# Performance work log

Measured on AMD Instinct MI355X. Metric: run time of the kernel, lower is better.

The kernel has to match this reference:

```python
import jax, jax.numpy as jnp
import numpy as np

B, N, IN_DIM, DIM, HEADS, P = 4, 2048, 256, 512, 8, 16
DH = DIM // HEADS            # 64
SCALE = DH ** -0.5


def setup_inputs() -> dict:
    key = jax.random.key(0)
    ks = jax.random.split(key, 8)
    def w(k, shape, s=0.02):
        return jax.random.normal(k, shape, dtype=jnp.float32) * s
    return {
        "x": jax.random.normal(ks[0], (B, N, IN_DIM), dtype=jnp.float32),
        "w_qkv": w(ks[1], (IN_DIM, 3 * DIM)),
        "b_qkv": jnp.zeros((3 * DIM,), jnp.float32),
        "w_in": w(ks[2], (P, P)),
        "b_in": jnp.zeros((P,), jnp.float32),
        "w_out": w(ks[3], (P, P)),
        "b_out": jnp.zeros((P,), jnp.float32),
        "w_merge": w(ks[4], (DIM, DIM)),
        "b_merge": jnp.zeros((DIM,), jnp.float32),
        "w_proj": w(ks[5], (DIM + IN_DIM, DIM)),
        "b_proj": jnp.zeros((DIM,), jnp.float32),
        "H": 64,
        "W": 32,
    }


def reference(x, w_qkv, b_qkv, w_in, b_in, w_out, b_out,
              w_merge, b_merge, w_proj, b_proj, H, W):
    b, n, _ = x.shape
    qkv = x @ w_qkv + b_qkv                      # [b, n, 3*DIM]
    q, k, v = jnp.split(qkv, 3, axis=-1)
    def to_heads(t):
        return t.reshape(b, n, HEADS, DH).transpose(0, 2, 1, 3)  # [b, h, n, d]
    q, k, v = to_heads(q), to_heads(k), to_heads(v)
    # Original splits heads into h/v halves and runs two attentions, then
    # concats along the head axis. Softmax is per-head, so this is exactly
    # one batched multi-head attention with head order preserved.
    attn = jax.nn.softmax(jnp.einsum('bhnd,bhmd->bhnm', q, k) * SCALE, axis=-1)
    out = jnp.einsum('bhnm,bhmd->bhnd', attn, v)
    out = out.transpose(0, 2, 1, 3).reshape(b, n, DIM)
    out = out @ w_merge + b_merge
    # IBPP branch: view channels as [P, P] grid, linear-SiLU-linear on last dim
    xr = x.reshape(b, n, P, P)
    ib = jax.nn.silu(xr @ w_in + b_in) @ w_out + b_out
    ib = ib.reshape(b, n, IN_DIM)
    # proj (dropout p=0 -> identity)
    return jnp.concatenate([out, ib], axis=-1) @ w_proj + b_proj
```

## Files before the change

kernel.cpp:

```cpp
#include <hip/hip_runtime.h>


typedef unsigned short u16;
typedef unsigned int u32;
typedef __bf16 bf16x8 __attribute__((ext_vector_type(8)));
typedef u16 su16x8 __attribute__((ext_vector_type(8)));
typedef u16 su16x4 __attribute__((ext_vector_type(4)));
typedef u32 u32x4 __attribute__((ext_vector_type(4)));
typedef float f32x4 __attribute__((ext_vector_type(4)));

__device__ __forceinline__ u16 f2bf(float f) {
  union { __bf16 h; u16 u; } v;
  v.h = (__bf16)f;
  return v.u;
}

__device__ __forceinline__ float fexp2(float x) {
#if __has_builtin(__builtin_amdgcn_exp2f)
  return __builtin_amdgcn_exp2f(x);
#else
  return __expf(x * 0.6931471805599453f);
#endif
}

__device__ __forceinline__ f32x4 zero4() {
  f32x4 v = {0.f, 0.f, 0.f, 0.f};
  return v;
}

__device__ __forceinline__ f32x4 mfma16(bf16x8 a, bf16x8 b, f32x4 c) {
  return __builtin_amdgcn_mfma_f32_16x16x32_bf16(a, b, c, 0, 0, 0);
}

__global__ __launch_bounds__(256) void prep_kernel(
    const float* __restrict__ w_qkv, const float* __restrict__ w_merge,
    const float* __restrict__ w_proj, const float* __restrict__ b_merge,
    const float* __restrict__ b_proj, u16* __restrict__ wqkvT,
    u16* __restrict__ wptT, u16* __restrict__ wcombT, u16* __restrict__ wmb,
    float* __restrict__ biasc) {
  int blk = blockIdx.x, tid = threadIdx.x;
  if (blk < 192) {
    const float* src;
    int lsrc, ldd, r0, c0;
    u16* dst;
    if (blk < 96) {
      src = w_qkv; lsrc = 1536; dst = wqkvT; ldd = 256;
      r0 = (blk & 3) * 64; c0 = (blk >> 2) * 64;
    } else if (blk < 160) {
      int b2 = blk - 96;
      src = w_proj; lsrc = 512; dst = wptT; ldd = 512;
      r0 = (b2 & 7) * 64; c0 = (b2 >> 3) * 64;
    } else {
      int b2 = blk - 160;
      src = w_proj + 512 * 512; lsrc = 512; dst = wcombT + 512; ldd = 768;
      r0 = (b2 & 3) * 64; c0 = (b2 >> 2) * 64;
    }
    __shared__ __align__(16) u16 Ts[64 * 68];
    int rr = tid >> 4, cc4 = (tid & 15) * 4;
#pragma unroll
    for (int rep = 0; rep < 4; ++rep) {
      int r = rr + rep * 16;
      float4 v = *(const float4*)&src[(size_t)(r0 + r) * lsrc + c0 + cc4];
      su16x4 pk = {f2bf(v.x), f2bf(v.y), f2bf(v.z), f2bf(v.w)};
      *(su16x4*)&Ts[r * 68 + cc4] = pk;
    }
    __syncthreads();
    int c = tid & 63, seg = tid >> 6;
    u16 tmp[16];
#pragma unroll
    for (int k = 0; k < 16; ++k) tmp[k] = Ts[(seg * 16 + k) * 68 + c];
    *(su16x8*)&dst[(size_t)(c0 + c) * ldd + r0 + seg * 16] = *(su16x8*)tmp;
    *(su16x8*)&dst[(size_t)(c0 + c) * ldd + r0 + seg * 16 + 8] =
        *(su16x8*)(tmp + 8);
  } else if (blk < 256) {
    int b2 = blk - 192;
#pragma unroll
    for (int rep = 0; rep < 4; ++rep) {
      int i = b2 * 4096 + rep * 1024 + tid * 4;
      float4 v = *(const float4*)&w_merge[i];
      su16x4 pk = {f2bf(v.x), f2bf(v.y), f2bf(v.z), f2bf(v.w)};
      *(su16x4*)&wmb[i] = pk;
    }
  } else {
    int col0 = (blk - 256) * 16;
    __shared__ float red[16][17];
    int kr = tid >> 4, cc = tid & 15;
    float s = 0.f;
#pragma unroll 4
    for (int j = 0; j < 32; ++j) {
      int k = kr + j * 16;
      s += b_merge[k] * w_proj[(size_t)k * 512 + col0 + cc];
    }
    red[kr][cc] = s;
    __syncthreads();
    if (kr == 0) {
      float a = b_proj[col0 + cc];
#pragma unroll
      for (int t = 0; t < 16; ++t) a += red[t][cc];
      biasc[col0 + cc] = a;
    }
  }
}

__global__ __launch_bounds__(256) void ib_kernel(
    const float* __restrict__ x, const float* __restrict__ w_in,
    const float* __restrict__ b_in, const float* __restrict__ w_out,
    const float* __restrict__ b_out, u16* __restrict__ xb,
    u16* __restrict__ catb) {
  __shared__ float wi[256], wo[256], bi[16], bo[16];
  __shared__ float xs[16][260];
  __shared__ float hs[16][260];
  int tid = threadIdx.x;
  wi[tid] = w_in[tid];
  wo[tid] = w_out[tid];
  if (tid < 16) { bi[tid] = b_in[tid]; bo[tid] = b_out[tid]; }
  size_t blkoff = (size_t)blockIdx.x * 4096;
#pragma unroll
  for (int i = 0; i < 4; ++i) {
    int f = (tid + i * 256) * 4;
    float4 v = *(const float4*)&x[blkoff + f];
    int tok = f >> 8, p = f & 255;
    *(float4*)&xs[tok][p] = v;
    su16x4 pk = {f2bf(v.x), f2bf(v.y), f2bf(v.z), f2bf(v.w)};
    *(su16x4*)&xb[blkoff + f] = pk;
  }
  __syncthreads();
  int t = tid >> 4, p2 = tid & 15;
#pragma unroll
  for (int p1 = 0; p1 < 16; ++p1) {
    float a = bi[p2];
#pragma unroll
    for (int k = 0; k < 16; ++k) a += xs[t][p1 * 16 + k] * wi[k * 16 + p2];
    hs[t][p1 * 16 + p2] = a / (1.f + __expf(-a));
  }
  __syncthreads();
  size_t tok = (size_t)blockIdx.x * 16 + t;
#pragma unroll
  for (int p1 = 0; p1 < 16; ++p1) {
    float o = bo[p2];
#pragma unroll
    for (int j = 0; j < 16; ++j) o += hs[t][p1 * 16 + j] * wo[j * 16 + p2];
    catb[tok * 768 + 512 + p1 * 16 + p2] = f2bf(o);
  }
}

template <int TM, int TN, int WGM, int WGN, int OUTMODE>
__global__ __launch_bounds__(256) void gemm_bt(
    const u16* __restrict__ A, int lda, const u16* __restrict__ BT, int ldb,
    int kcount, const float* __restrict__ bias, void* __restrict__ Co, int ldc,
    int scaleQ) {
  constexpr int NROWS = TM + TN;
  constexpr int NLD = NROWS / 64;
  constexpr int MT = TM / WGM / 16;
  constexpr int NT = TN / WGN / 16;
  __shared__ __align__(16) u16 S[NROWS * 40];
  int tid = threadIdx.x;
  int lane = tid & 63, wave = tid >> 6;
  int c = lane & 15, g4 = lane >> 4;
  int m0 = blockIdx.y * TM, n0 = blockIdx.x * TN;
  int wm = (wave / WGN) * (TM / WGM), wn = (wave % WGN) * (TN / WGN);
  f32x4 acc[MT][NT];
#pragma unroll
  for (int a = 0; a < MT; ++a)
#pragma unroll
    for (int b = 0; b < NT; ++b) acc[a][b] = zero4();

  su16x8 pre[NLD];
#pragma unroll
  for (int t = 0; t < NLD; ++t) {
    int gsl = t * 256 + tid;
    int row = gsl >> 2, kg = gsl & 3;
    const u16* p = row < TM ? &A[(size_t)(m0 + row) * lda + kg * 8]
                            : &BT[(size_t)(n0 + row - TM) * ldb + kg * 8];
    pre[t] = *(const su16x8*)p;
  }

  for (int kb = 0; kb < kcount; kb += 32) {
    __syncthreads();
#pragma unroll
    for (int t = 0; t < NLD; ++t) {
      int gsl = t * 256 + tid;
      int row = gsl >> 2, kg = gsl & 3;
      *(su16x8*)&S[row * 40 + kg * 8] = pre[t];
    }
    __syncthreads();
    if (kb + 32 < kcount) {
#pragma unroll
      for (int t = 0; t < NLD; ++t) {
        int gsl = t * 256 + tid;
        int row = gsl >> 2, kg = gsl & 3;
        const u16* p =
            row < TM ? &A[(size_t)(m0 + row) * lda + kb + 32 + kg * 8]
                     : &BT[(size_t)(n0 + row - TM) * ldb + kb + 32 + kg * 8];
        pre[t] = *(const su16x8*)p;
      }
    }
    bf16x8 af[MT], bf[NT];
#pragma unroll
    for (int mt = 0; mt < MT; ++mt)
      af[mt] = *(const bf16x8*)&S[(wm + mt * 16 + c) * 40 + g4 * 8];
#pragma unroll
    for (int nt = 0; nt < NT; ++nt)
      bf[nt] = *(const bf16x8*)&S[(TM + wn + nt * 16 + c) * 40 + g4 * 8];
#pragma unroll
    for (int mt = 0; mt < MT; ++mt)
#pragma unroll
      for (int nt = 0; nt < NT; ++nt)
        acc[mt][nt] = mfma16(af[mt], bf[nt], acc[mt][nt]);
  }

  if (OUTMODE == 0) {
    float* Cf = (float*)Co;
#pragma unroll
    for (int nt = 0; nt < NT; ++nt) {
      int col = n0 + wn + nt * 16 + c;
      float bv = bias ? bias[col] : 0.f;
#pragma unroll
      for (int mt = 0; mt < MT; ++mt)
#pragma unroll
        for (int i = 0; i < 4; ++i)
          Cf[(size_t)(m0 + wm + mt * 16 + g4 * 4 + i) * ldc + col] =
              acc[mt][nt][i] + bv;
    }
  } else if (OUTMODE == 2) {
    u16* C16 = (u16*)Co;
#pragma unroll
    for (int nt = 0; nt < NT; ++nt)
#pragma unroll
      for (int mt = 0; mt < MT; ++mt)
#pragma unroll
        for (int i = 0; i < 4; ++i)
          C16[(size_t)(m0 + wm + mt * 16 + g4 * 4 + i) * ldc + n0 + wn +
              nt * 16 + c] = f2bf(acc[mt][nt][i]);
  } else {
    u16* C16 = (u16*)Co;
    u16* Cs = S;
    __syncthreads();
#pragma unroll
    for (int half = 0; half < 2; ++half) {
      if ((wave >> 1) == half) {
#pragma unroll
        for (int nt = 0; nt < NT; ++nt) {
          int col = n0 + wn + nt * 16 + c;
          float bv = bias ? bias[col] : 0.f;
          float sc = (scaleQ && col < 512) ? 0.18033688011112042f : 1.f;
#pragma unroll
          for (int mt = 0; mt < MT; ++mt)
#pragma unroll
            for (int i = 0; i < 4; ++i)
              Cs[(mt * 16 + g4 * 4 + i) * 136 + wn + nt * 16 + c] =
                  f2bf((acc[mt][nt][i] + bv) * sc);
        }
      }
      __syncthreads();
      {
        int row = tid >> 2;
#pragma unroll
        for (int t = 0; t < 4; ++t) {
          int gr = (tid & 3) + t * 4;
          u32x4 v = *(const u32x4*)&Cs[row * 136 + gr * 8];
          *(u32x4*)&C16[(size_t)(m0 + half * 64 + row) * ldc + n0 + gr * 8] = v;
        }
      }
      __syncthreads();
    }
  }
}

__global__ __launch_bounds__(256) void attn_kernel(
    const u16* __restrict__ qkvb, u16* __restrict__ catb) {
  __shared__ __align__(16) u16 Ks[9216];
  __shared__ __align__(16) u16 Vs[8704];
  __shared__ __align__(16) u16 Ps[8704];
  int tid = threadIdx.x;
  int lane = tid & 63, wave = tid >> 6;
  int c = lane & 15, g4 = lane >> 4;
  int wq = wave * 32;
  int bh = blockIdx.x & 31, qt = blockIdx.x >> 5;
  int bb = bh >> 3, h = bh & 7;
  size_t base = (size_t)bb * 2048 * 1536;
  u16* Psw = Ps + wave * (16 * 136);

  bf16x8 qf[2][2];
#pragma unroll
  for (int qt2 = 0; qt2 < 2; ++qt2)
#pragma unroll
    for (int ks2 = 0; ks2 < 2; ++ks2) {
      int n = qt * 128 + wq + qt2 * 16 + c;
      qf[qt2][ks2] = *(const bf16x8*)&qkvb[base + (size_t)n * 1536 + h * 64 +
                                           ks2 * 32 + g4 * 8];
    }
  f32x4 oacc[2][4];
#pragma unroll
  for (int a = 0; a < 2; ++a)
#pragma unroll
    for (int b = 0; b < 4; ++b) oacc[a][b] = zero4();
  float lsum[2] = {0.f, 0.f};

  su16x8 kpre[4], v0pre[2], v1pre[2];
  int kv_s = tid >> 3, dg_s = tid & 7;

  auto loadKV = [&](int n0k) {
#pragma unroll
    for (int t = 0; t < 4; ++t)
      kpre[t] = *(const su16x8*)&qkvb[base + (size_t)(n0k + kv_s + t * 32) *
                                                1536 +
                                      512 + h * 64 + dg_s * 8];
#pragma unroll
    for (int t = 0; t < 2; ++t) {
      const u16* vg = &qkvb[base + (size_t)(n0k + (kv_s + t * 32) * 2) * 1536 +
                            1024 + h * 64 + dg_s * 8];
      v0pre[t] = *(const su16x8*)vg;
      v1pre[t] = *(const su16x8*)(vg + 1536);
    }
  };

  loadKV(0);
  for (int kb2 = 0; kb2 < 16; ++kb2) {
    __syncthreads();
#pragma unroll
    for (int t = 0; t < 4; ++t)
      *(su16x8*)&Ks[(kv_s + t * 32) * 72 + dg_s * 8] = kpre[t];
#pragma unroll
    for (int t = 0; t < 2; ++t) {
      int kvp = kv_s + t * 32;
      u32* vw = (u32*)Vs;
      int kvg = kvp >> 2, w2 = kvp & 3;
#pragma unroll
      for (int j = 0; j < 8; ++j) {
        int d = dg_s * 8 + j;
        vw[d * 68 + ((kvg ^ (dg_s & 3)) << 2) + w2] =
            (u32)v0pre[t][j] | ((u32)v1pre[t][j] << 16);
      }
    }
    __syncthreads();
    if (kb2 < 15) loadKV((kb2 + 1) * 128);
    f32x4 sacc[2][8];
#pragma unroll
    for (int a = 0; a < 2; ++a)
#pragma unroll
      for (int b = 0; b < 8; ++b) sacc[a][b] = zero4();
#pragma unroll
    for (int ks2 = 0; ks2 < 2; ++ks2)
#pragma unroll
      for (int kvt = 0; kvt < 8; ++kvt) {
        bf16x8 kf = *(const bf16x8*)&Ks[(kvt * 16 + c) * 72 + ks2 * 32 + g4 * 8];
        sacc[0][kvt] = mfma16(kf, qf[0][ks2], sacc[0][kvt]);
        sacc[1][kvt] = mfma16(kf, qf[1][ks2], sacc[1][kvt]);
      }
    bf16x8 pf[2][4];
#pragma unroll
    for (int qt2 = 0; qt2 < 2; ++qt2) {
      float part = 0.f;
#pragma unroll
      for (int kvt = 0; kvt < 8; ++kvt) {
        float p0 = fexp2(sacc[qt2][kvt][0]);
        float p1 = fexp2(sacc[qt2][kvt][1]);
        float p2 = fexp2(sacc[qt2][kvt][2]);
        float p3 = fexp2(sacc[qt2][kvt][3]);
        part += (p0 + p1) + (p2 + p3);
        su16x4 pk = {f2bf(p0), f2bf(p1), f2bf(p2), f2bf(p3)};
        *(su16x4*)&Psw[c * 136 + kvt * 16 + g4 * 4] = pk;
      }
      lsum[qt2] += part;
#pragma unroll
      for (int ks = 0; ks < 4; ++ks)
        pf[qt2][ks] = *(const bf16x8*)&Psw[c * 136 + ks * 32 + g4 * 8];
    }
#pragma unroll
    for (int ks = 0; ks < 4; ++ks)
#pragma unroll
      for (int nt = 0; nt < 4; ++nt) {
        int d = nt * 16 + c;
        bf16x8 vf = *(const bf16x8*)&Vs[d * 136 +
                                        (((ks * 4 + g4) ^ ((d >> 3) & 3)) << 3)];
        oacc[0][nt] = mfma16(pf[0][ks], vf, oacc[0][nt]);
        oacc[1][nt] = mfma16(pf[1][ks], vf, oacc[1][nt]);
      }
  }
#pragma unroll
  for (int qt2 = 0; qt2 < 2; ++qt2) {
    lsum[qt2] += __shfl_xor(lsum[qt2], 16);
    lsum[qt2] += __shfl_xor(lsum[qt2], 32);
  }
#pragma unroll
  for (int qt2 = 0; qt2 < 2; ++qt2) {
    float linv[4];
#pragma unroll
    for (int i = 0; i < 4; ++i)
      linv[i] = 1.f / __shfl(lsum[qt2], g4 * 4 + i);
#pragma unroll
    for (int nt = 0; nt < 4; ++nt)
#pragma unroll
      for (int i = 0; i < 4; ++i) {
        int n = qt * 128 + wq + qt2 * 16 + g4 * 4 + i;
        catb[(size_t)(bb * 2048 + n) * 768 + h * 64 + nt * 16 + c] =
            f2bf(oacc[qt2][nt][i] * linv[i]);
      }
  }
}

extern "C" void kernel_launch(void* const* d_in, const int* in_sizes, int n_in,
                              void* d_out, int out_size, void* d_ws,
                              size_t ws_size, hipStream_t stream) {
  const float* x = (const float*)d_in[0];
  const float* w_qkv = (const float*)d_in[1];
  const float* b_qkv = (const float*)d_in[2];
  const float* w_in = (const float*)d_in[3];
  const float* b_in = (const float*)d_in[4];
  const float* w_out = (const float*)d_in[5];
  const float* b_out = (const float*)d_in[6];
  const float* w_merge = (const float*)d_in[7];
  const float* b_merge = (const float*)d_in[8];
  const float* w_proj = (const float*)d_in[9];
  const float* b_proj = (const float*)d_in[10];

  char* ws = (char*)d_ws;
  u16* xb = (u16*)(ws + 0);
  u16* qkvb = (u16*)(ws + 4194304);
  u16* catb = (u16*)(ws + 29360128);
  u16* wqkvT = (u16*)(ws + 41943040);
  u16* wptT = (u16*)(ws + 42729472);
  u16* wmb = (u16*)(ws + 43253760);
  u16* wcombT = (u16*)(ws + 43778048);
  float* biasc = (float*)(ws + 44564480);

  prep_kernel<<<288, 256, 0, stream>>>(w_qkv, w_merge, w_proj, b_merge, b_proj,
                                       wqkvT, wptT, wcombT, wmb, biasc);
  ib_kernel<<<512, 256, 0, stream>>>(x, w_in, b_in, w_out, b_out, xb, catb);
  gemm_bt<128, 128, 2, 2, 1><<<dim3(12, 64), 256, 0, stream>>>(
      xb, 256, wqkvT, 256, 256, b_qkv, (void*)qkvb, 1536, 1);
  gemm_bt<64, 64, 2, 2, 2><<<dim3(8, 8), 256, 0, stream>>>(
      wptT, 512, wmb, 512, 512, nullptr, (void*)wcombT, 768, 0);
  attn_kernel<<<512, 256, 0, stream>>>(qkvb, catb);
  gemm_bt<128, 64, 4, 1, 0><<<dim3(8, 64), 256, 0, stream>>>(
      catb, 768, wcombT, 768, 768, biasc, d_out, 512, 0);
}
```

Measured before the change: 191.1 us.

## Rewrite attention inner loop with 32x32 MFMA, in-register P, double-buffered K/V

```diff
diff --git a/kernel.cpp b/kernel.cpp
--- a/kernel.cpp
+++ b/kernel.cpp
@@ -8,6 +8,7 @@
 typedef u16 su16x4 __attribute__((ext_vector_type(4)));
 typedef u32 u32x4 __attribute__((ext_vector_type(4)));
 typedef float f32x4 __attribute__((ext_vector_type(4)));
+typedef float f32x16 __attribute__((ext_vector_type(16)));
 
 __device__ __forceinline__ u16 f2bf(float f) {
   union { __bf16 h; u16 u; } v;
@@ -30,6 +31,26 @@
 
 __device__ __forceinline__ f32x4 mfma16(bf16x8 a, bf16x8 b, f32x4 c) {
   return __builtin_amdgcn_mfma_f32_16x16x32_bf16(a, b, c, 0, 0, 0);
+}
+
+__device__ __forceinline__ f32x16 mfma32(bf16x8 a, bf16x8 b, f32x16 c) {
+  return __builtin_amdgcn_mfma_f32_32x32x16_bf16(a, b, c, 0, 0, 0);
+}
+
+__device__ __forceinline__ u32 pkbf(float a, float b) {
+  u32 r;
+  asm("v_cvt_pk_bf16_f32 %0, %1, %2" : "=v"(r) : "v"(a), "v"(b));
+  return r;
+}
+
+__device__ __forceinline__ void swap32(u32& a, u32& b) {
+  asm("v_permlane32_swap_b32 %0, %1" : "+v"(a), "+v"(b));
+}
+
+__device__ __forceinline__ bf16x8 mkfrag(u32 w0, u32 w1, u32 w2, u32 w3) {
+  union { u32 u[4]; bf16x8 v; } x;
+  x.u[0] = w0; x.u[1] = w1; x.u[2] = w2; x.u[3] = w3;
+  return x.v;
 }
 
 __global__ __launch_bounds__(256) void prep_kernel(
@@ -267,35 +288,32 @@
   }
 }
 
-__global__ __launch_bounds__(256) void attn_kernel(
+__global__ __launch_bounds__(256, 2) void attn_kernel(
     const u16* __restrict__ qkvb, u16* __restrict__ catb) {
-  __shared__ __align__(16) u16 Ks[9216];
-  __shared__ __align__(16) u16 Vs[8704];
-  __shared__ __align__(16) u16 Ps[8704];
+  __shared__ __align__(16) u16 Ks[2 * 9216];
+  __shared__ __align__(16) u16 Vs[2 * 8704];
   int tid = threadIdx.x;
   int lane = tid & 63, wave = tid >> 6;
-  int c = lane & 15, g4 = lane >> 4;
+  int l31 = lane & 31, hi = lane >> 5;
   int wq = wave * 32;
   int bh = blockIdx.x & 31, qt = blockIdx.x >> 5;
   int bb = bh >> 3, h = bh & 7;
   size_t base = (size_t)bb * 2048 * 1536;
-  u16* Psw = Ps + wave * (16 * 136);
-
-  bf16x8 qf[2][2];
-#pragma unroll
-  for (int qt2 = 0; qt2 < 2; ++qt2)
-#pragma unroll
-    for (int ks2 = 0; ks2 < 2; ++ks2) {
-      int n = qt * 128 + wq + qt2 * 16 + c;
-      qf[qt2][ks2] = *(const bf16x8*)&qkvb[base + (size_t)n * 1536 + h * 64 +
-                                           ks2 * 32 + g4 * 8];
-    }
-  f32x4 oacc[2][4];
-#pragma unroll
-  for (int a = 0; a < 2; ++a)
-#pragma unroll
-    for (int b = 0; b < 4; ++b) oacc[a][b] = zero4();
-  float lsum[2] = {0.f, 0.f};
+
+  bf16x8 qf[4];
+  {
+    int n = qt * 128 + wq + l31;
+    const u16* qp = &qkvb[base + (size_t)n * 1536 + h * 64 + hi * 8];
+#pragma unroll
+    for (int kc = 0; kc < 4; ++kc) qf[kc] = *(const bf16x8*)(qp + kc * 16);
+  }
+
+  f32x16 oacc[2];
+#pragma unroll
+  for (int dt = 0; dt < 2; ++dt)
+#pragma unroll
+    for (int r = 0; r < 16; ++r) oacc[dt][r] = 0.f;
+  float lsum = 0.f;
 
   su16x8 kpre[4], v0pre[2], v1pre[2];
   int kv_s = tid >> 3, dg_s = tid & 7;
@@ -315,16 +333,15 @@
     }
   };
 
-  loadKV(0);
-  for (int kb2 = 0; kb2 < 16; ++kb2) {
-    __syncthreads();
+  auto stage = [&](int buf) {
+    u16* ksw = Ks + buf * 9216;
+    u32* vw = (u32*)(Vs + buf * 8704);
 #pragma unroll
     for (int t = 0; t < 4; ++t)
-      *(su16x8*)&Ks[(kv_s + t * 32) * 72 + dg_s * 8] = kpre[t];
+      *(su16x8*)&ksw[(kv_s + t * 32) * 72 + dg_s * 8] = kpre[t];
 #pragma unroll
     for (int t = 0; t < 2; ++t) {
       int kvp = kv_s + t * 32;
-      u32* vw = (u32*)Vs;
       int kvg = kvp >> 2, w2 = kvp & 3;
 #pragma unroll
       for (int j = 0; j < 8; ++j) {
@@ -333,70 +350,72 @@
             (u32)v0pre[t][j] | ((u32)v1pre[t][j] << 16);
       }
     }
-    __syncthreads();
+  };
+
+  loadKV(0);
+  stage(0);
+  for (int kb2 = 0; kb2 < 16; ++kb2) {
+    __syncthreads();
+    int cur = kb2 & 1;
     if (kb2 < 15) loadKV((kb2 + 1) * 128);
-    f32x4 sacc[2][8];
-#pragma unroll
-    for (int a = 0; a < 2; ++a)
-#pragma unroll
-      for (int b = 0; b < 8; ++b) sacc[a][b] = zero4();
-#pragma unroll
-    for (int ks2 = 0; ks2 < 2; ++ks2)
-#pragma unroll
-      for (int kvt = 0; kvt < 8; ++kvt) {
-        bf16x8 kf = *(const bf16x8*)&Ks[(kvt * 16 + c) * 72 + ks2 * 32 + g4 * 8];
-        sacc[0][kvt] = mfma16(kf, qf[0][ks2], sacc[0][kvt]);
-        sacc[1][kvt] = mfma16(kf, qf[1][ks2], sacc[1][kvt]);
+    const u16* ksb = Ks + cur * 9216;
+    const u16* vsb = Vs + cur * 8704;
+#pragma unroll
+    for (int kvt = 0; kvt < 4; ++kvt) {
+      bf16x8 kf[4];
+#pragma unroll
+      for (int kc = 0; kc < 4; ++kc)
+        kf[kc] =
+            *(const bf16x8*)&ksb[(kvt * 32 + l31) * 72 + kc * 16 + hi * 8];
+      f32x16 sacc;
+#pragma unroll
+      for (int r = 0; r < 16; ++r) sacc[r] = 0.f;
+      __builtin_amdgcn_s_setprio(1);
+#pragma unroll
+      for (int kc = 0; kc < 4; ++kc) sacc = mfma32(kf[kc], qf[kc], sacc);
+      __builtin_amdgcn_s_setprio(0);
+      float p[16];
+#pragma unroll
+      for (int r = 0; r < 16; ++r) p[r] = fexp2(sacc[r]);
+      lsum += ((((p[0] + p[1]) + (p[2] + p[3])) +
+                ((p[4] + p[5]) + (p[6] + p[7]))) +
+               (((p[8] + p[9]) + (p[10] + p[11])) +
+                ((p[12] + p[13]) + (p[14] + p[15]))));
+      u32 a0 = pkbf(p[0], p[1]), b0 = pkbf(p[4], p[5]);
+      u32 a1 = pkbf(p[2], p[3]), b1 = pkbf(p[6], p[7]);
+      u32 a2 = pkbf(p[8], p[9]), b2 = pkbf(p[12], p[13]);
+      u32 a3 = pkbf(p[10], p[11]), b3 = pkbf(p[14], p[15]);
+      swap32(a0, b0);
+      swap32(a1, b1);
+      swap32(a2, b2);
+      swap32(a3, b3);
+      bf16x8 pf0 = mkfrag(a0, a1, b0, b1);
+      bf16x8 pf1 = mkfrag(a2, a3, b2, b3);
+      __builtin_amdgcn_s_setprio(1);
+#pragma unroll
+      for (int kc2 = 0; kc2 < 2; ++kc2) {
+        int g = (kvt * 2 + kc2) * 2 + hi;
+#pragma unroll
+        for (int dt = 0; dt < 2; ++dt) {
+          int d = dt * 32 + l31;
+          bf16x8 vf =
+              *(const bf16x8*)&vsb[d * 136 + ((g ^ ((d >> 3) & 3)) << 3)];
+          oacc[dt] = mfma32(kc2 ? pf1 : pf0, vf, oacc[dt]);
+        }
       }
-    bf16x8 pf[2][4];
-#pragma unroll
-    for (int qt2 = 0; qt2 < 2; ++qt2) {
-      float part = 0.f;
-#pragma unroll
-      for (int kvt = 0; kvt < 8; ++kvt) {
-        float p0 = fexp2(sacc[qt2][kvt][0]);
-        float p1 = fexp2(sacc[qt2][kvt][1]);
-        float p2 = fexp2(sacc[qt2][kvt][2]);
-        float p3 = fexp2(sacc[qt2][kvt][3]);
-        part += (p0 + p1) + (p2 + p3);
-        su16x4 pk = {f2bf(p0), f2bf(p1), f2bf(p2), f2bf(p3)};
-        *(su16x4*)&Psw[c * 136 + kvt * 16 + g4 * 4] = pk;
-      }
-      lsum[qt2] += part;
-#pragma unroll
-      for (int ks = 0; ks < 4; ++ks)
-        pf[qt2][ks] = *(const bf16x8*)&Psw[c * 136 + ks * 32 + g4 * 8];
-    }
-#pragma unroll
-    for (int ks = 0; ks < 4; ++ks)
-#pragma unroll
-      for (int nt = 0; nt < 4; ++nt) {
-        int d = nt * 16 + c;
-        bf16x8 vf = *(const bf16x8*)&Vs[d * 136 +
-                                        (((ks * 4 + g4) ^ ((d >> 3) & 3)) << 3)];
-        oacc[0][nt] = mfma16(pf[0][ks], vf, oacc[0][nt]);
-        oacc[1][nt] = mfma16(pf[1][ks], vf, oacc[1][nt]);
-      }
-  }
-#pragma unroll
-  for (int qt2 = 0; qt2 < 2; ++qt2) {
-    lsum[qt2] += __shfl_xor(lsum[qt2], 16);
-    lsum[qt2] += __shfl_xor(lsum[qt2], 32);
-  }
-#pragma unroll
-  for (int qt2 = 0; qt2 < 2; ++qt2) {
-    float linv[4];
-#pragma unroll
-    for (int i = 0; i < 4; ++i)
-      linv[i] = 1.f / __shfl(lsum[qt2], g4 * 4 + i);
-#pragma unroll
-    for (int nt = 0; nt < 4; ++nt)
-#pragma unroll
-      for (int i = 0; i < 4; ++i) {
-        int n = qt * 128 + wq + qt2 * 16 + g4 * 4 + i;
-        catb[(size_t)(bb * 2048 + n) * 768 + h * 64 + nt * 16 + c] =
-            f2bf(oacc[qt2][nt][i] * linv[i]);
-      }
+      __builtin_amdgcn_s_setprio(0);
+    }
+    if (kb2 < 15) stage(cur ^ 1);
+  }
+  lsum += __shfl_xor(lsum, 32);
+#pragma unroll
+  for (int r = 0; r < 16; ++r) {
+    int qrow = (r & 3) + 8 * (r >> 2) + 4 * hi;
+    float linv = 1.f / __shfl(lsum, qrow);
+    size_t n = (size_t)(bb * 2048 + qt * 128 + wq + qrow);
+    u16* cp = &catb[n * 768 + h * 64];
+    cp[l31] = f2bf(oacc[0][r] * linv);
+    cp[32 + l31] = f2bf(oacc[1][r] * linv);
   }
 }
 
```

After: 182.7 us. 4.4% less time.
